# Kernel optimization log

Measured on AMD Instinct MI355X. Metric: run time of the kernel, lower is better.

Reference implementation:

```python
import jax, jax.numpy as jnp
import numpy as np

N_HEADS = 4

def _conv2d(x, w, b):
    # NCHW input, OIHW weight, 3x3 SAME, stride 1
    y = jax.lax.conv_general_dilated(x, w, window_strides=(1, 1), padding='SAME',
                                     dimension_numbers=('NCHW', 'OIHW', 'NCHW'))
    return y + b[None, :, None, None]


def setup_inputs() -> dict:
    key = jax.random.key(0)
    ks = jax.random.split(key, 5)
    x = jax.random.normal(ks[0], (4, 32, 256, 256), dtype=jnp.float32)
    conv1_w = jax.random.normal(ks[1], (384, 32, 3, 3), dtype=jnp.float32) * 0.05
    conv1_b = jax.random.normal(ks[2], (384,), dtype=jnp.float32) * 0.05
    conv2_w = jax.random.normal(ks[3], (32, 128, 3, 3), dtype=jnp.float32) * 0.05
    conv2_b = jax.random.normal(ks[4], (32,), dtype=jnp.float32) * 0.05
    return {'x': x, 'conv1_w': conv1_w, 'conv1_b': conv1_b,
            'conv2_w': conv2_w, 'conv2_b': conv2_b}


def reference(x, conv1_w, conv1_b, conv2_w, conv2_b):
    b, c_in, h, w = x.shape
    n = h * w
    qkv = _conv2d(x, conv1_w, conv1_b)              # [b, 3*heads*d, h, w]
    d = qkv.shape[1] // (3 * N_HEADS)               # head dim
    qkv = qkv.reshape(b, 3, N_HEADS, d, n)          # 'b (qkv heads c) h w -> b qkv heads c n'
    q, k, v = qkv[:, 0], qkv[:, 1], qkv[:, 2]
    k = jax.nn.softmax(k, axis=-1)                  # softmax over n = h*w
    weights = jnp.einsum('bhdn,bhen->bhde', q, k)   # [b, heads, d, d] context
    out = jnp.einsum('bhde,bhdn->bhen', weights, v) # [b, heads, d, n]
    out = out.reshape(b, N_HEADS * d, h, w)         # 'b heads c n -> b (heads c) h w'
    return _conv2d(out, conv2_w, conv2_b)
```

## Files before the change

### kernel.cpp

```cpp
#include <hip/hip_runtime.h>
#include <hip/hip_bf16.h>

typedef __hip_bfloat16 bf16;
typedef __attribute__((ext_vector_type(8))) short short8;
typedef __attribute__((ext_vector_type(4))) float f32x4;
typedef __attribute__((ext_vector_type(16))) float f32x16;

#define B_    4
#define CIN   32
#define HH    256
#define WW    256
#define C1    384
#define NPIX  65536
#define CMID  128
#define COUT  32
#define PW    258

static __device__ __forceinline__ float u2f(unsigned short u) {
    unsigned int x = ((unsigned int)u) << 16;
    return __uint_as_float(x);
}
static __device__ __forceinline__ unsigned short f2u(float f) {
    bf16 h = __float2bfloat16(f);
    return __builtin_bit_cast(unsigned short, h);
}
static __device__ __forceinline__ unsigned int pk2(float lo, float hi) {
    return (unsigned int)f2u(lo) | ((unsigned int)f2u(hi) << 16);
}
static __device__ __forceinline__ void gload16(const void* src, void* dst) {
    __builtin_amdgcn_global_load_lds(
        (const __attribute__((address_space(1))) void*)src,
        (__attribute__((address_space(3))) void*)dst, 16, 0, 0);
}

__global__ __launch_bounds__(256) void k_w1t(const float* __restrict__ w1, short* __restrict__ w1t) {
    const int tap = blockIdx.x;
    for (int i = threadIdx.x; i < 384 * 32; i += 256) {
        int co = i >> 5, cij = i & 31;
        w1t[((size_t)(tap * 4 + (cij >> 3)) * 384 + co) * 8 + (cij & 7)] =
            (short)f2u(w1[(size_t)i * 9 + tap]);
    }
}
__global__ __launch_bounds__(256) void k_w2t(const float* __restrict__ w2, short* __restrict__ w2t) {
    const int tap = blockIdx.x;
    for (int i = threadIdx.x; i < 32 * 128; i += 256) {
        int co = i >> 7, cij = i & 127;
        w2t[((size_t)(tap * 16 + (cij >> 3)) * 32 + co) * 8 + (cij & 7)] =
            (short)f2u(w2[(size_t)i * 9 + tap]);
    }
}

__global__ __launch_bounds__(256) void k_xt2(const float* __restrict__ x,
                                             unsigned short* __restrict__ xt2, int b0) {
    const int row = blockIdx.x, bl = blockIdx.y, b = b0 + bl;
    const int tx = threadIdx.x;
    unsigned short* rbase = xt2 + (size_t)(bl * PW + row) * 4 * PW * 8;
    const uint4 z = make_uint4(0u, 0u, 0u, 0u);
    if (row == 0 || row == PW - 1) {
        for (int i = tx; i < 4 * PW; i += 256) ((uint4*)rbase)[i] = z;
        return;
    }
    if (tx < 2) {
        int c = tx ? (PW - 1) : 0;
#pragma unroll
        for (int ch = 0; ch < 4; ch++)
            *(uint4*)(rbase + ((size_t)ch * PW + c) * 8) = z;
    }
    const int col = tx + 1;
    const size_t px = (size_t)(row - 1) * WW + tx;
    unsigned int pk[16];
#pragma unroll
    for (int c2 = 0; c2 < 16; c2++) {
        float v0 = x[((size_t)b * CIN + 2 * c2) * NPIX + px];
        float v1 = x[((size_t)b * CIN + 2 * c2 + 1) * NPIX + px];
        pk[c2] = pk2(v0, v1);
    }
#pragma unroll
    for (int ch = 0; ch < 4; ch++)
        *(uint4*)(rbase + ((size_t)ch * PW + col) * 8) =
            make_uint4(pk[ch * 4], pk[ch * 4 + 1], pk[ch * 4 + 2], pk[ch * 4 + 3]);
}

__global__ __launch_bounds__(256, 3) void k_conv1(
    const unsigned short* __restrict__ xt2, const short* __restrict__ w1t,
    const float* __restrict__ b1, unsigned short* __restrict__ vt,
    float* __restrict__ pw, float* __restrict__ ps, int nb)
{
    const int nblk = 512 * nb;
    const int m = ((int)blockIdx.x & 7) * (nblk >> 3) + ((int)blockIdx.x >> 3);
    const int chunk = m & 1;
    const int y   = (m >> 1) & 255;
    const int bl  = m >> 9;
    const int px0 = chunk * 128;
    const int cid = bl * 512 + y * 2 + chunk;
    const int tx  = threadIdx.x;
    const int wv  = tx >> 6, l = tx & 63;
    const int lhi = l >> 4, llo = l & 15;

    __shared__ short xs[12 * 132 * 8];
    __shared__ union {
        short os[64][136];
        short ost[128][66];
        float osw[4][32][32];
    } ou;

#pragma unroll
    for (int i = 0; i < 3; i++) {
        int p = wv * 3 + i;
        int r = p >> 2, ch = p & 3;
        const char* src = (const char*)xt2 +
            (((size_t)(bl * PW) + y + r) * 4 + ch) * (PW * 16) + (size_t)px0 * 16 + (size_t)l * 16;
        char* dst = (char*)xs + p * 2112;
        gload16(src, dst);
        gload16(src + 1024, dst + 1024);
        if (l < 2) gload16(src + 2048, dst + 2048);
    }
    __syncthreads();

    const short* wbase = w1t + ((size_t)lhi * 384 + llo) * 8;

    short8 qa[2][4];
    f32x4 wacc[2][2];
#pragma unroll
    for (int dt = 0; dt < 2; dt++)
#pragma unroll
        for (int et = 0; et < 2; et++) wacc[dt][et] = (f32x4){0.f, 0.f, 0.f, 0.f};
    float se0 = 0.f, se1 = 0.f;

#pragma unroll
    for (int cog = 0; cog < 6; cog++) {
        const int co0 = cog * 64;

        f32x4 acc[2][4];
#pragma unroll
        for (int t = 0; t < 2; t++)
#pragma unroll
            for (int mc = 0; mc < 4; mc++) acc[t][mc] = (f32x4){0.f, 0.f, 0.f, 0.f};

        short8 a[4], an[4];
#pragma unroll
        for (int mc = 0; mc < 4; mc++)
            an[mc] = *(const short8*)(wbase + ((size_t)co0 + mc * 16) * 8);
#pragma unroll
        for (int tap = 0; tap < 9; tap++) {
            const int dy = tap / 3, dx = tap % 3;
#pragma unroll
            for (int mc = 0; mc < 4; mc++) a[mc] = an[mc];
            if (tap < 8) {
#pragma unroll
                for (int mc = 0; mc < 4; mc++)
                    an[mc] = *(const short8*)(wbase +
                        ((size_t)(tap + 1) * 4 * 384 + co0 + mc * 16) * 8);
            }
#pragma unroll
            for (int t = 0; t < 2; t++) {
                short8 bfr = *(const short8*)&xs[(((dy * 4 + lhi) * 132) + (wv * 32 + t * 16 + llo + dx)) * 8];
#pragma unroll
                for (int mc = 0; mc < 4; mc++)
                    acc[t][mc] = __builtin_amdgcn_mfma_f32_16x16x32_bf16(a[mc], bfr, acc[t][mc], 0, 0, 0);
            }
        }

        float bias[4][4];
#pragma unroll
        for (int mc = 0; mc < 4; mc++)
#pragma unroll
            for (int r = 0; r < 4; r++)
                bias[mc][r] = b1[co0 + mc * 16 + lhi * 4 + r];

        __syncthreads();

        if (cog < 4) {
#pragma unroll
            for (int t = 0; t < 2; t++)
#pragma unroll
                for (int mc = 0; mc < 4; mc++)
#pragma unroll
                    for (int r = 0; r < 4; r++)
                        ou.os[mc * 16 + lhi * 4 + r][wv * 32 + t * 16 + llo] =
                            (short)f2u(acc[t][mc][r] + bias[mc][r]);
        } else {
#pragma unroll
            for (int t = 0; t < 2; t++)
#pragma unroll
                for (int mc = 0; mc < 4; mc++)
#pragma unroll
                    for (int r = 0; r < 4; r++)
                        ou.ost[wv * 32 + t * 16 + llo][mc * 16 + lhi * 4 + r] =
                            (short)f2u(acc[t][mc][r] + bias[mc][r]);
        }
        __syncthreads();

        if (cog < 2) {
            if ((wv >> 1) == cog) {
                const int chb = (wv & 1) * 32;
#pragma unroll
                for (int dt = 0; dt < 2; dt++)
#pragma unroll
                    for (int ks = 0; ks < 4; ks++)
                        qa[dt][ks] = *(const short8*)&ou.os[chb + dt * 16 + llo][ks * 32 + lhi * 8];
            }
        } else if (cog < 4) {
            if ((wv >> 1) == cog - 2) {
                const int chb = (wv & 1) * 32;
#pragma unroll
                for (int et = 0; et < 2; et++)
#pragma unroll
                    for (int ks = 0; ks < 4; ks++) {
                        short8 kf = *(const short8*)&ou.os[chb + et * 16 + llo][ks * 32 + lhi * 8];
                        short8 pf;
#pragma unroll
                        for (int j = 0; j < 8; j++) {
                            float ef = __expf(u2f((unsigned short)kf[j]));
                            if (et == 0) se0 += ef; else se1 += ef;
                            pf[j] = (short)f2u(ef);
                        }
#pragma unroll
                        for (int dt = 0; dt < 2; dt++)
                            wacc[dt][et] = __builtin_amdgcn_mfma_f32_16x16x32_bf16(
                                qa[dt][ks], pf, wacc[dt][et], 0, 0, 0);
                    }
            }
        } else {
            unsigned short* dst = vt + ((size_t)(bl * 2 + (cog - 4)) * NPIX
                                        + y * WW + px0) * 64;
#pragma unroll
            for (int i = 0; i < 4; i++) {
                int u = i * 256 + tx;
                int px = u >> 3, q = u & 7;
                uint4 v = *(const uint4*)&ou.ost[px][q * 8];
                *(uint4*)(dst + (size_t)u * 8) = v;
            }
        }
    }

    se0 += __shfl_xor(se0, 16); se0 += __shfl_xor(se0, 32);
    se1 += __shfl_xor(se1, 16); se1 += __shfl_xor(se1, 32);
    if (l < 16) {
        ps[(size_t)cid * 128 + wv * 32 + llo]      = se0;
        ps[(size_t)cid * 128 + wv * 32 + 16 + llo] = se1;
    }

    __syncthreads();
#pragma unroll
    for (int dt = 0; dt < 2; dt++)
#pragma unroll
        for (int et = 0; et < 2; et++)
#pragma unroll
            for (int r = 0; r < 4; r++)
                ou.osw[wv][dt * 16 + lhi * 4 + r][et * 16 + llo] = wacc[dt][et][r];
    __syncthreads();

    {
        float* pwp = pw + (size_t)cid * 4096;
        const float* osf = (const float*)&ou;
#pragma unroll
        for (int p = 0; p < 4; p++)
            *(float4*)(pwp + p * 1024 + tx * 4) = *(const float4*)(osf + p * 1024 + tx * 4);
    }
}

__global__ __launch_bounds__(256) void k_wred(
    const float* __restrict__ pw, const float* __restrict__ ps,
    float* __restrict__ wts, int b0)
{
    const int bh = blockIdx.x;
    const int jq = blockIdx.y;
    const int bl = bh >> 2, h = bh & 3;
    const int tx = threadIdx.x;
    __shared__ float rinvs[32];
    if (tx < 32) {
        float s = 0.f;
        const float* pp = ps + (size_t)bl * 512 * 128 + h * 32 + tx;
        for (int c = 0; c < 512; c++) s += pp[(size_t)c * 128];
        rinvs[tx] = 1.f / s;
    }
    __syncthreads();
    const int i = jq * 256 + tx;
    const float* pwp = pw + (size_t)bl * 512 * 4096 + h * 1024 + i;
    float s = 0.f;
    for (int c = 0; c < 512; c++) s += pwp[(size_t)c * 4096];
    wts[(size_t)(b0 * 4 + bh) * 1024 + i] = s * rinvs[i & 31];
}

__global__ __launch_bounds__(256, 3) void k_conv2f(
    const unsigned short* __restrict__ vt, const short* __restrict__ w2t,
    const float* __restrict__ wts, const float* __restrict__ b2,
    float* __restrict__ out, int b0, int nb)
{
    const int nblk = 512 * nb;
    const int m = ((int)blockIdx.x & 7) * (nblk >> 3) + ((int)blockIdx.x >> 3);
    const int chunk = m & 1;
    const int y   = (m >> 1) & 255;
    const int bl  = m >> 9;
    const int px0 = chunk * 128;
    const int bb  = b0 + bl;
    const int tx  = threadIdx.x;
    const int wv  = tx >> 6, l = tx & 63;
    const int lhi = l >> 4, llo = l & 15;

    __shared__ short xs[12 * 137 * 8];
    __shared__ float osf[32][132];
    __shared__ short wtsb[4][2][64][8];

    for (int i = tx; i < 4096; i += 256) {
        int h = i >> 10, r = i & 1023;
        int kh = r >> 9, s = r & 511, li = s >> 3, j = s & 7;
        int d = kh * 16 + (li >> 5) * 8 + j, e = li & 31;
        wtsb[h][kh][li][j] = (short)f2u(wts[(size_t)bb * 4096 + h * 1024 + d * 32 + e]);
    }

    float bias[2][4];
#pragma unroll
    for (int mm = 0; mm < 2; mm++)
#pragma unroll
        for (int r = 0; r < 4; r++)
            bias[mm][r] = b2[mm * 16 + lhi * 4 + r];

    f32x4 acc[2][2];
#pragma unroll
    for (int t = 0; t < 2; t++)
#pragma unroll
        for (int mm = 0; mm < 2; mm++) acc[t][mm] = (f32x4){0.f, 0.f, 0.f, 0.f};

    __syncthreads();

    const int kg = l >> 5;
    const int pxa = l & 31;

    for (int cc = 0; cc < 4; cc++) {
        const int plane = cc >> 1, chofs = (cc & 1) * 32;
        short8 B0 = *(const short8*)&wtsb[cc][0][l][0];
        short8 B1 = *(const short8*)&wtsb[cc][1][l][0];

        for (int idx = wv; idx < 15; idx += 4) {
            int rr = idx / 5, ti = idx % 5;
            int ar = y - 1 + rr;
            int colbase = (ti < 4) ? ti * 32 : 99;
            if (ar < 0 || ar > 255) {
#pragma unroll
                for (int r = 0; r < 16; r++) {
                    int pxl = (r & 3) + 8 * (r >> 2) + 4 * kg;
                    int e = pxa;
                    xs[(((rr * 4 + (e >> 3)) * 137) + colbase + pxl) * 8 + (e & 7)] = 0;
                }
            } else {
                int ac = px0 - 1 + colbase + pxa;
                short8 A0 = (short8){0,0,0,0,0,0,0,0};
                short8 A1 = (short8){0,0,0,0,0,0,0,0};
                if (ac >= 0 && ac < 256) {
                    const unsigned short* vp = vt +
                        ((size_t)(bl * 2 + plane) * NPIX + (size_t)ar * 256 + ac) * 64
                        + chofs + kg * 8;
                    A0 = *(const short8*)vp;
                    A1 = *(const short8*)(vp + 16);
                }
                f32x16 aa;
#pragma unroll
                for (int r = 0; r < 16; r++) aa[r] = 0.f;
                aa = __builtin_amdgcn_mfma_f32_32x32x16_bf16(A0, B0, aa, 0, 0, 0);
                aa = __builtin_amdgcn_mfma_f32_32x32x16_bf16(A1, B1, aa, 0, 0, 0);
#pragma unroll
                for (int r = 0; r < 16; r++) {
                    int pxl = (r & 3) + 8 * (r >> 2) + 4 * kg;
                    int e = pxa;
                    xs[(((rr * 4 + (e >> 3)) * 137) + colbase + pxl) * 8 + (e & 7)] =
                        (short)f2u(aa[r]);
                }
            }
        }
        __syncthreads();

        short8 a[2], an[2];
#pragma unroll
        for (int mm = 0; mm < 2; mm++)
            an[mm] = *(const short8*)(w2t + ((size_t)(cc * 4 + lhi) * 32 + mm * 16 + llo) * 8);
#pragma unroll
        for (int tap = 0; tap < 9; tap++) {
            const int dy = tap / 3, dx = tap % 3;
#pragma unroll
            for (int mm = 0; mm < 2; mm++) a[mm] = an[mm];
            if (tap < 8) {
#pragma unroll
                for (int mm = 0; mm < 2; mm++)
                    an[mm] = *(const short8*)(w2t +
                        ((size_t)((tap + 1) * 16 + cc * 4 + lhi) * 32 + mm * 16 + llo) * 8);
            }
#pragma unroll
            for (int t = 0; t < 2; t++) {
                short8 bfr = *(const short8*)&xs[(((dy * 4 + lhi) * 137) + (wv * 32 + t * 16 + llo + dx)) * 8];
#pragma unroll
                for (int mm = 0; mm < 2; mm++)
                    acc[t][mm] = __builtin_amdgcn_mfma_f32_16x16x32_bf16(a[mm], bfr, acc[t][mm], 0, 0, 0);
            }
        }
        __syncthreads();
    }

#pragma unroll
    for (int t = 0; t < 2; t++)
#pragma unroll
        for (int mm = 0; mm < 2; mm++)
#pragma unroll
            for (int r = 0; r < 4; r++)
                osf[mm * 16 + lhi * 4 + r][wv * 32 + t * 16 + llo] = acc[t][mm][r] + bias[mm][r];
    __syncthreads();
#pragma unroll
    for (int p = 0; p < 4; p++) {
        int chl = p * 8 + (tx >> 5);
        float4 v = *(const float4*)&osf[chl][(tx & 31) * 4];
        *(float4*)(out + ((size_t)bb * COUT + chl) * NPIX + y * WW + px0 + (tx & 31) * 4) = v;
    }
}

extern "C" void kernel_launch(void* const* d_in, const int* in_sizes, int n_in,
                              void* d_out, int out_size, void* d_ws, size_t ws_size,
                              hipStream_t stream) {
    const float* x  = (const float*)d_in[0];
    const float* w1 = (const float*)d_in[1];
    const float* b1 = (const float*)d_in[2];
    const float* w2 = (const float*)d_in[3];
    const float* b2 = (const float*)d_in[4];
    float* out = (float*)d_out;

    char* ws = (char*)d_ws;
    float* wts  = (float*)(ws + 4096);
    short* w1t  = (short*)(ws + 69632);
    short* w2t  = (short*)(ws + 290816);
    const size_t OFF_XT = 1048576;

    int nb = 4;
    size_t xt_sz = (size_t)nb * PW * 4 * PW * 16;
    size_t pw_sz = (size_t)nb * 512 * 4096 * 4;
    size_t ps_sz = (size_t)nb * 512 * 128 * 4;
    size_t vt_sz = (size_t)nb * 2 * NPIX * 64 * 2;
    if (ws_size < OFF_XT + xt_sz + pw_sz + ps_sz + vt_sz) {
        nb = 1;
        xt_sz = (size_t)nb * PW * 4 * PW * 16;
        pw_sz = (size_t)nb * 512 * 4096 * 4;
        ps_sz = (size_t)nb * 512 * 128 * 4;
        vt_sz = (size_t)nb * 2 * NPIX * 64 * 2;
    }
    const size_t pw_off = OFF_XT + xt_sz;
    const size_t ps_off = pw_off + pw_sz;
    const size_t vt_off = ps_off + ps_sz;

    unsigned short* xt2 = (unsigned short*)(ws + OFF_XT);
    float*          pw  = (float*)(ws + pw_off);
    float*          psb = (float*)(ws + ps_off);
    unsigned short* vt  = (unsigned short*)(ws + vt_off);

    k_w1t<<<dim3(9), 256, 0, stream>>>(w1, w1t);
    k_w2t<<<dim3(9), 256, 0, stream>>>(w2, w2t);

    for (int b0 = 0; b0 < B_; b0 += nb) {
        k_xt2  <<<dim3(PW, nb),      256, 0, stream>>>(x, xt2, b0);
        k_conv1<<<dim3(2 * HH * nb), 256, 0, stream>>>(xt2, w1t, b1, vt, pw, psb, nb);
        k_wred <<<dim3(nb * 4, 4),   256, 0, stream>>>(pw, psb, wts, b0);
        k_conv2f<<<dim3(2 * HH * nb),256, 0, stream>>>(vt, w2t, wts, b2, out, b0, nb);
    }
}
```

Before: 197.0 us.

## Fold attention context into conv2 weights and pad V layout for direct LDS loads

The per-batch context matrix is folded into the conv2 weights by a new small kernel, so conv2 no longer runs an MFMA context transform per tile of V. V is written into a zero-bordered padded layout, which lets conv2 fill its halo tile with async global-to-LDS loads instead of computing it. The partial context sums are also stored as bf16 to halve that traffic. The bf16 rounding of the partial sums and of the fused weights adds precision risk.

Result: no change. 197.2 us (+0.1%).

```diff
diff --git a/kernel.cpp b/kernel.cpp
--- a/kernel.cpp
+++ b/kernel.cpp
@@ -15,6 +15,7 @@
 #define CMID  128
 #define COUT  32
 #define PW    258
+#define VROW  16512
 
 static __device__ __forceinline__ float u2f(unsigned short u) {
     unsigned int x = ((unsigned int)u) << 16;
@@ -39,14 +40,6 @@
         int co = i >> 5, cij = i & 31;
         w1t[((size_t)(tap * 4 + (cij >> 3)) * 384 + co) * 8 + (cij & 7)] =
             (short)f2u(w1[(size_t)i * 9 + tap]);
-    }
-}
-__global__ __launch_bounds__(256) void k_w2t(const float* __restrict__ w2, short* __restrict__ w2t) {
-    const int tap = blockIdx.x;
-    for (int i = threadIdx.x; i < 32 * 128; i += 256) {
-        int co = i >> 7, cij = i & 127;
-        w2t[((size_t)(tap * 16 + (cij >> 3)) * 32 + co) * 8 + (cij & 7)] =
-            (short)f2u(w2[(size_t)i * 9 + tap]);
     }
 }
 
@@ -81,10 +74,22 @@
             make_uint4(pk[ch * 4], pk[ch * 4 + 1], pk[ch * 4 + 2], pk[ch * 4 + 3]);
 }
 
+__global__ __launch_bounds__(256) void k_bordv(unsigned short* __restrict__ vt) {
+    const int row = blockIdx.x, bp = blockIdx.y, tx = threadIdx.x;
+    unsigned short* base = vt + ((size_t)bp * PW + row) * VROW;
+    const uint4 z = make_uint4(0u, 0u, 0u, 0u);
+    if (row == 0 || row == PW - 1) {
+        for (int i = tx; i < VROW / 8; i += 256) ((uint4*)base)[i] = z;
+    } else if (tx < 16) {
+        int g = tx >> 1, c = (tx & 1) * (PW - 1);
+        *(uint4*)(base + ((size_t)g * PW + c) * 8) = z;
+    }
+}
+
 __global__ __launch_bounds__(256, 3) void k_conv1(
     const unsigned short* __restrict__ xt2, const short* __restrict__ w1t,
     const float* __restrict__ b1, unsigned short* __restrict__ vt,
-    float* __restrict__ pw, float* __restrict__ ps, int nb)
+    unsigned short* __restrict__ pw, float* __restrict__ ps, int nb)
 {
     const int nblk = 512 * nb;
     const int m = ((int)blockIdx.x & 7) * (nblk >> 3) + ((int)blockIdx.x >> 3);
@@ -101,7 +106,7 @@
     __shared__ union {
         short os[64][136];
         short ost[128][66];
-        float osw[4][32][32];
+        short osw[4][32][32];
     } ou;
 
 #pragma unroll
@@ -222,14 +227,14 @@
                     }
             }
         } else {
-            unsigned short* dst = vt + ((size_t)(bl * 2 + (cog - 4)) * NPIX
-                                        + y * WW + px0) * 64;
+            const int plane = cog - 4;
+            unsigned short* rowb = vt + ((size_t)(bl * 2 + plane) * PW + 1 + y) * VROW;
 #pragma unroll
             for (int i = 0; i < 4; i++) {
                 int u = i * 256 + tx;
-                int px = u >> 3, q = u & 7;
-                uint4 v = *(const uint4*)&ou.ost[px][q * 8];
-                *(uint4*)(dst + (size_t)u * 8) = v;
+                int g = u >> 7, px = u & 127;
+                uint4 v = *(const uint4*)&ou.ost[px][g * 8];
+                *(uint4*)(rowb + ((size_t)g * PW + 1 + px0 + px) * 8) = v;
             }
         }
     }
@@ -248,20 +253,20 @@
         for (int et = 0; et < 2; et++)
 #pragma unroll
             for (int r = 0; r < 4; r++)
-                ou.osw[wv][dt * 16 + lhi * 4 + r][et * 16 + llo] = wacc[dt][et][r];
+                ou.osw[wv][dt * 16 + lhi * 4 + r][et * 16 + llo] = (short)f2u(wacc[dt][et][r]);
     __syncthreads();
 
     {
-        float* pwp = pw + (size_t)cid * 4096;
-        const float* osf = (const float*)&ou;
-#pragma unroll
-        for (int p = 0; p < 4; p++)
-            *(float4*)(pwp + p * 1024 + tx * 4) = *(const float4*)(osf + p * 1024 + tx * 4);
+        unsigned short* pwp = pw + (size_t)cid * 4096;
+        const unsigned short* osf = (const unsigned short*)&ou;
+#pragma unroll
+        for (int p = 0; p < 2; p++)
+            *(uint4*)(pwp + p * 2048 + tx * 8) = *(const uint4*)(osf + p * 2048 + tx * 8);
     }
 }
 
 __global__ __launch_bounds__(256) void k_wred(
-    const float* __restrict__ pw, const float* __restrict__ ps,
+    const unsigned short* __restrict__ pw, const float* __restrict__ ps,
     float* __restrict__ wts, int b0)
 {
     const int bh = blockIdx.x;
@@ -277,16 +282,43 @@
     }
     __syncthreads();
     const int i = jq * 256 + tx;
-    const float* pwp = pw + (size_t)bl * 512 * 4096 + h * 1024 + i;
+    const unsigned short* pwp = pw + (size_t)bl * 512 * 4096 + h * 1024 + i;
     float s = 0.f;
-    for (int c = 0; c < 512; c++) s += pwp[(size_t)c * 4096];
+    for (int c = 0; c < 512; c++) s += u2f(pwp[(size_t)c * 4096]);
     wts[(size_t)(b0 * 4 + bh) * 1024 + i] = s * rinvs[i & 31];
 }
 
-__global__ __launch_bounds__(256, 3) void k_conv2f(
-    const unsigned short* __restrict__ vt, const short* __restrict__ w2t,
-    const float* __restrict__ wts, const float* __restrict__ b2,
-    float* __restrict__ out, int b0, int nb)
+__global__ __launch_bounds__(256) void k_w2e(
+    const float* __restrict__ w2, const float* __restrict__ wts,
+    short* __restrict__ w2te, int b0)
+{
+    const int bl = blockIdx.x, tap = blockIdx.y;
+    const int tx = threadIdx.x;
+    __shared__ float Wsh[4096];
+    __shared__ float w2sh[4096];
+    for (int i = tx; i < 4096; i += 256) {
+        Wsh[i]  = wts[(size_t)(b0 + bl) * 4096 + i];
+        w2sh[i] = w2[(size_t)i * 9 + tap];
+    }
+    __syncthreads();
+#pragma unroll
+    for (int rep = 0; rep < 16; rep++) {
+        int o = rep * 256 + tx;
+        int cv = o >> 5, co = o & 31;
+        int h = cv >> 5, d = cv & 31;
+        const float* wp = &w2sh[co * 128 + 32 * h];
+        const float* Wp = &Wsh[h * 1024 + d * 32];
+        float s = 0.f;
+#pragma unroll
+        for (int e = 0; e < 32; e++) s += wp[e] * Wp[e];
+        w2te[((((size_t)bl * 9 + tap) * 16 + (cv >> 3)) * 32 + co) * 8 + (cv & 7)] =
+            (short)f2u(s);
+    }
+}
+
+__global__ __launch_bounds__(256, 3) void k_conv2e(
+    const unsigned short* __restrict__ vt, const short* __restrict__ w2te,
+    const float* __restrict__ b2, float* __restrict__ out, int b0, int nb)
 {
     const int nblk = 512 * nb;
     const int m = ((int)blockIdx.x & 7) * (nblk >> 3) + ((int)blockIdx.x >> 3);
@@ -299,16 +331,10 @@
     const int wv  = tx >> 6, l = tx & 63;
     const int lhi = l >> 4, llo = l & 15;
 
-    __shared__ short xs[12 * 137 * 8];
+    __shared__ short xs[12 * 132 * 8];
     __shared__ float osf[32][132];
-    __shared__ short wtsb[4][2][64][8];
-
-    for (int i = tx; i < 4096; i += 256) {
-        int h = i >> 10, r = i & 1023;
-        int kh = r >> 9, s = r & 511, li = s >> 3, j = s & 7;
-        int d = kh * 16 + (li >> 5) * 8 + j, e = li & 31;
-        wtsb[h][kh][li][j] = (short)f2u(wts[(size_t)bb * 4096 + h * 1024 + d * 32 + e]);
-    }
+
+    const short* w2b = w2te + (size_t)bl * 9 * 16 * 32 * 8;
 
     float bias[2][4];
 #pragma unroll
@@ -323,58 +349,27 @@
 #pragma unroll
         for (int mm = 0; mm < 2; mm++) acc[t][mm] = (f32x4){0.f, 0.f, 0.f, 0.f};
 
-    __syncthreads();
-
-    const int kg = l >> 5;
-    const int pxa = l & 31;
-
     for (int cc = 0; cc < 4; cc++) {
-        const int plane = cc >> 1, chofs = (cc & 1) * 32;
-        short8 B0 = *(const short8*)&wtsb[cc][0][l][0];
-        short8 B1 = *(const short8*)&wtsb[cc][1][l][0];
-
-        for (int idx = wv; idx < 15; idx += 4) {
-            int rr = idx / 5, ti = idx % 5;
-            int ar = y - 1 + rr;
-            int colbase = (ti < 4) ? ti * 32 : 99;
-            if (ar < 0 || ar > 255) {
-#pragma unroll
-                for (int r = 0; r < 16; r++) {
-                    int pxl = (r & 3) + 8 * (r >> 2) + 4 * kg;
-                    int e = pxa;
-                    xs[(((rr * 4 + (e >> 3)) * 137) + colbase + pxl) * 8 + (e & 7)] = 0;
-                }
-            } else {
-                int ac = px0 - 1 + colbase + pxa;
-                short8 A0 = (short8){0,0,0,0,0,0,0,0};
-                short8 A1 = (short8){0,0,0,0,0,0,0,0};
-                if (ac >= 0 && ac < 256) {
-                    const unsigned short* vp = vt +
-                        ((size_t)(bl * 2 + plane) * NPIX + (size_t)ar * 256 + ac) * 64
-                        + chofs + kg * 8;
-                    A0 = *(const short8*)vp;
-                    A1 = *(const short8*)(vp + 16);
-                }
-                f32x16 aa;
-#pragma unroll
-                for (int r = 0; r < 16; r++) aa[r] = 0.f;
-                aa = __builtin_amdgcn_mfma_f32_32x32x16_bf16(A0, B0, aa, 0, 0, 0);
-                aa = __builtin_amdgcn_mfma_f32_32x32x16_bf16(A1, B1, aa, 0, 0, 0);
-#pragma unroll
-                for (int r = 0; r < 16; r++) {
-                    int pxl = (r & 3) + 8 * (r >> 2) + 4 * kg;
-                    int e = pxa;
-                    xs[(((rr * 4 + (e >> 3)) * 137) + colbase + pxl) * 8 + (e & 7)] =
-                        (short)f2u(aa[r]);
-                }
-            }
+        const int plane = cc >> 1, ghalf = cc & 1;
+        __syncthreads();
+#pragma unroll
+        for (int i = 0; i < 3; i++) {
+            int p = wv * 3 + i;
+            int r = p >> 2, sg = p & 3;
+            const char* src = (const char*)vt +
+                (((size_t)(bl * 2 + plane) * PW + y + r) * VROW
+                 + ((size_t)(ghalf * 4 + sg) * PW + px0) * 8) * 2 + (size_t)l * 16;
+            char* dst = (char*)xs + p * 2112;
+            gload16(src, dst);
+            gload16(src + 1024, dst + 1024);
+            if (l < 2) gload16(src + 2048, dst + 2048);
         }
         __syncthreads();
 
         short8 a[2], an[2];
 #pragma unroll
         for (int mm = 0; mm < 2; mm++)
-            an[mm] = *(const short8*)(w2t + ((size_t)(cc * 4 + lhi) * 32 + mm * 16 + llo) * 8);
+            an[mm] = *(const short8*)(w2b + ((size_t)(cc * 4 + lhi) * 32 + mm * 16 + llo) * 8);
 #pragma unroll
         for (int tap = 0; tap < 9; tap++) {
             const int dy = tap / 3, dx = tap % 3;
@@ -383,18 +378,17 @@
             if (tap < 8) {
 #pragma unroll
                 for (int mm = 0; mm < 2; mm++)
-                    an[mm] = *(const short8*)(w2t +
+                    an[mm] = *(const short8*)(w2b +
                         ((size_t)((tap + 1) * 16 + cc * 4 + lhi) * 32 + mm * 16 + llo) * 8);
             }
 #pragma unroll
             for (int t = 0; t < 2; t++) {
-                short8 bfr = *(const short8*)&xs[(((dy * 4 + lhi) * 137) + (wv * 32 + t * 16 + llo + dx)) * 8];
+                short8 bfr = *(const short8*)&xs[(((dy * 4 + lhi) * 132) + (wv * 32 + t * 16 + llo + dx)) * 8];
 #pragma unroll
                 for (int mm = 0; mm < 2; mm++)
                     acc[t][mm] = __builtin_amdgcn_mfma_f32_16x16x32_bf16(a[mm], bfr, acc[t][mm], 0, 0, 0);
             }
         }
-        __syncthreads();
     }
 
 #pragma unroll
@@ -426,37 +420,38 @@
     char* ws = (char*)d_ws;
     float* wts  = (float*)(ws + 4096);
     short* w1t  = (short*)(ws + 69632);
-    short* w2t  = (short*)(ws + 290816);
+    short* w2te = (short*)(ws + 364544);
     const size_t OFF_XT = 1048576;
 
     int nb = 4;
     size_t xt_sz = (size_t)nb * PW * 4 * PW * 16;
-    size_t pw_sz = (size_t)nb * 512 * 4096 * 4;
+    size_t pw_sz = (size_t)nb * 512 * 4096 * 2;
     size_t ps_sz = (size_t)nb * 512 * 128 * 4;
-    size_t vt_sz = (size_t)nb * 2 * NPIX * 64 * 2;
+    size_t vt_sz = (size_t)nb * 2 * PW * (size_t)VROW * 2;
     if (ws_size < OFF_XT + xt_sz + pw_sz + ps_sz + vt_sz) {
         nb = 1;
         xt_sz = (size_t)nb * PW * 4 * PW * 16;
-        pw_sz = (size_t)nb * 512 * 4096 * 4;
+        pw_sz = (size_t)nb * 512 * 4096 * 2;
         ps_sz = (size_t)nb * 512 * 128 * 4;
-        vt_sz = (size_t)nb * 2 * NPIX * 64 * 2;
+        vt_sz = (size_t)nb * 2 * PW * (size_t)VROW * 2;
     }
     const size_t pw_off = OFF_XT + xt_sz;
     const size_t ps_off = pw_off + pw_sz;
     const size_t vt_off = ps_off + ps_sz;
 
     unsigned short* xt2 = (unsigned short*)(ws + OFF_XT);
-    float*          pw  = (float*)(ws + pw_off);
+    unsigned short* pw  = (unsigned short*)(ws + pw_off);
     float*          psb = (float*)(ws + ps_off);
     unsigned short* vt  = (unsigned short*)(ws + vt_off);
 
     k_w1t<<<dim3(9), 256, 0, stream>>>(w1, w1t);
-    k_w2t<<<dim3(9), 256, 0, stream>>>(w2, w2t);
 
     for (int b0 = 0; b0 < B_; b0 += nb) {
         k_xt2  <<<dim3(PW, nb),      256, 0, stream>>>(x, xt2, b0);
+        k_bordv<<<dim3(PW, nb * 2),  256, 0, stream>>>(vt);
         k_conv1<<<dim3(2 * HH * nb), 256, 0, stream>>>(xt2, w1t, b1, vt, pw, psb, nb);
         k_wred <<<dim3(nb * 4, 4),   256, 0, stream>>>(pw, psb, wts, b0);
-        k_conv2f<<<dim3(2 * HH * nb),256, 0, stream>>>(vt, w2t, wts, b2, out, b0, nb);
-    }
-}
+        k_w2e  <<<dim3(nb, 9),       256, 0, stream>>>(w2, wts, w2te, b0);
+        k_conv2e<<<dim3(2 * HH * nb),256, 0, stream>>>(vt, w2te, b2, out, b0, nb);
+    }
+}
```
